# Kernel tuning notes

Measured on AMD Instinct MI355X. Metric: run time of the kernel, lower is better.

Reference implementation:

```python
import jax, jax.numpy as jnp
import numpy as np

IMG_TOK = 197  # hardcoded image/text split in the original module
BLOCK = 128


def setup_inputs() -> dict:
    key = jax.random.key(0)
    ks = jax.random.split(key, 11)
    B, Sk, Sv, D = 512, 128, 261, 768
    H, OUT = 58, 512
    return {
        "Q": jax.random.normal(ks[0], (B, D), jnp.float32),
        "K": jax.random.normal(ks[1], (B, Sk, D), jnp.float32),
        "V": jax.random.normal(ks[2], (B, Sv, D), jnp.float32),
        "Wq": jax.random.normal(ks[3], (H, D), jnp.float32) * 0.02,
        "bq": jax.random.normal(ks[4], (H,), jnp.float32) * 0.02,
        "Wk": jax.random.normal(ks[5], (H, D), jnp.float32) * 0.02,
        "bk": jax.random.normal(ks[6], (H,), jnp.float32) * 0.02,
        "Wsw": jax.random.normal(ks[7], (1, BLOCK), jnp.float32) * 0.02,
        "bsw": jax.random.normal(ks[8], (1,), jnp.float32) * 0.02,
        "Wv": jax.random.normal(ks[9], (OUT, D), jnp.float32) * 0.02,
        "bv": jax.random.normal(ks[10], (OUT,), jnp.float32) * 0.02,
    }


def reference(Q, K, V, Wq, bq, Wk, bk, Wsw, bsw, Wv, bv):
    Sk = K.shape[-2]
    # Linear projections (torch Linear: x @ W.T + b)
    Qt = Q[:, None, :] @ Wq.T + bq            # [B, 1, H]
    Kt = K @ Wk.T + bk                         # [B, Sk, H]
    Vt = V @ Wv.T + bv                         # [B, Sv, 512]
    # sigmoid attention over keys, scaled by sqrt(Sk)
    scores = jnp.einsum("bqh,bkh->bqk", Qt, Kt) / jnp.sqrt(jnp.float32(Sk))
    attn_weights = jax.nn.sigmoid(scores)      # [B, 1, Sk]
    # pad/truncate to BLOCK (no-op when Sk == BLOCK, matching original alignment)
    if attn_weights.shape[2] < BLOCK:
        attn_weights = jnp.pad(attn_weights, ((0, 0), (0, 0), (0, BLOCK - attn_weights.shape[2])))
    elif attn_weights.shape[2] > BLOCK:
        attn_weights = attn_weights[:, :, :BLOCK]
    # switch gate
    hot = jax.nn.sigmoid(attn_weights @ Wsw.T + bsw)   # [B, 1, 1]
    image_context = hot * Vt[:, :IMG_TOK, :]
    text_context = (1.0 - hot) * Vt[:, IMG_TOK:, :]
    context = jnp.concatenate((image_context, text_context), axis=1)  # [B, Sv, 512]
    return context, attn_weights
```

## Files before the change

kernel.cpp:

```cpp
#include <hip/hip_runtime.h>
#include <hip/hip_bf16.h>

constexpr int Bn   = 512;
constexpr int SK   = 128;
constexpr int SV   = 261;
constexpr int Dd   = 768;
constexpr int Hh   = 58;
constexpr int OUTn = 512;
constexpr int IMG  = 197;
constexpr int Mrows = Bn * SV;
constexpr long long CTX_ELEMS = (long long)Mrows * OUTn;

constexpr size_t WS_U   = 0;
constexpr size_t WS_C   = 1572864;
constexpr size_t WS_HOT = 1574912;
constexpr size_t WS_WB  = 1576960;

typedef __attribute__((ext_vector_type(8))) short short8;
typedef __attribute__((ext_vector_type(4))) float floatx4;

__device__ __forceinline__ short f2bf(float f) {
    return __builtin_bit_cast(short, __float2bfloat16(f));
}

__device__ __forceinline__ float sigmoidf_(float x) {
    return 1.0f / (1.0f + __expf(-x));
}

template <int N>
__device__ __forceinline__ void wait_vm() {
    asm volatile("s_waitcnt vmcnt(%0)" :: "n"(N) : "memory");
}

template <int OFF>
__device__ __forceinline__ floatx4 ds_read128(unsigned addr) {
    floatx4 r;
    asm volatile("ds_read_b128 %0, %1 offset:%2" : "=v"(r) : "v"(addr), "n"(OFF));
    return r;
}

__device__ __forceinline__ void lds_dma16(const float* src, float* dst) {
    __builtin_amdgcn_global_load_lds(
        (const __attribute__((address_space(1))) void*)src,
        (__attribute__((address_space(3))) void*)dst,
        16, 0, 0);
}

__global__ void __launch_bounds__(256) qt_u_kernel(
    const float* __restrict__ Q, const float* __restrict__ Wq, const float* __restrict__ bq,
    const float* __restrict__ Wk, const float* __restrict__ bk,
    float* __restrict__ u, float* __restrict__ c)
{
    int b = blockIdx.x;
    int t = threadIdx.x, lane = t & 63, w = t >> 6;

    __shared__ float qrow[Dd];
    __shared__ float qt[Hh];

    for (int d = t; d < Dd; d += 256) qrow[d] = Q[b * Dd + d];
    __syncthreads();

    for (int h = w; h < Hh; h += 4) {
        const float* wr = Wq + (size_t)h * Dd;
        float s = 0.f;
        #pragma unroll
        for (int j = 0; j < 12; ++j) { int d = lane + 64 * j; s += qrow[d] * wr[d]; }
        #pragma unroll
        for (int off = 32; off; off >>= 1) s += __shfl_down(s, off);
        if (lane == 0) qt[h] = s + bq[h];
    }
    __syncthreads();

    for (int d = t; d < Dd; d += 256) {
        float s = 0.f;
        #pragma unroll 2
        for (int h = 0; h < Hh; ++h) s += qt[h] * Wk[(size_t)h * Dd + d];
        u[(size_t)b * Dd + d] = s;
    }

    if (w == 0) {
        float v = (lane < Hh) ? qt[lane] * bk[lane] : 0.f;
        #pragma unroll
        for (int off = 32; off; off >>= 1) v += __shfl_down(v, off);
        if (lane == 0) c[b] = v;
    }
}

__global__ void __launch_bounds__(512) scores_kernel(
    const float* __restrict__ K, const float* __restrict__ u, const float* __restrict__ c,
    const float* __restrict__ Wsw, const float* __restrict__ bsw,
    float* __restrict__ attn_out, float* __restrict__ hot)
{
    int b = blockIdx.x;
    int t = threadIdx.x, lane = t & 63, w = t >> 6;

    __shared__ float ul[Dd];
    __shared__ float al[SK];

    for (int d = t; d < Dd; d += 512) ul[d] = u[(size_t)b * Dd + d];
    float cb = c[b];
    __syncthreads();

    const float* Kb = K + (size_t)b * SK * Dd;
    for (int k = w; k < SK; k += 8) {
        const float* kr = Kb + (size_t)k * Dd;
        float s = 0.f;
        #pragma unroll
        for (int j = 0; j < 12; ++j) { int d = lane + 64 * j; s += kr[d] * ul[d]; }
        #pragma unroll
        for (int off = 32; off; off >>= 1) s += __shfl_down(s, off);
        if (lane == 0) {
            float sc = (s + cb) * 0.0883883476483184f;
            float a = sigmoidf_(sc);
            attn_out[(size_t)b * SK + k] = a;
            al[k] = a;
        }
    }
    __syncthreads();

    if (w == 0) {
        float v = al[lane] * Wsw[lane] + al[lane + 64] * Wsw[lane + 64];
        #pragma unroll
        for (int off = 32; off; off >>= 1) v += __shfl_down(v, off);
        if (lane == 0) hot[b] = sigmoidf_(v + bsw[0]);
    }
}

__global__ void __launch_bounds__(256) wv_convert(
    const float* __restrict__ Wv, unsigned short* __restrict__ wsB)
{
    int t = blockIdx.x * 256 + threadIdx.x;
    if (t >= OUTn * Dd) return;
    int col = t / Dd;
    int k   = t - col * Dd;
    int kb = k >> 5, kgrp = (k >> 3) & 3, kj = k & 7;
    int g = col >> 4, cl = col & 15;
    size_t off = ((size_t)(kb * 32 + g) * 64 + (kgrp * 16 + cl)) * 8 + kj;
    wsB[off] = (unsigned short)f2bf(Wv[t]);
}

__global__ void __launch_bounds__(256, 2) ctx_gemm(
    const float* __restrict__ V, const unsigned short* __restrict__ wsB,
    const float* __restrict__ bv, const float* __restrict__ hot,
    float* __restrict__ out)
{
    int bid = blockIdx.x;
    int nt = bid & 1;
    int mt = bid >> 1;
    int t = threadIdx.x, lane = t & 63, w = t >> 6;
    int m_base = mt * 64;

    __shared__ float ldsA[3][2048];

    int r8 = lane >> 3;
    int glog = (lane & 7) ^ r8;
    const float* srcJ0 = V + (size_t)(m_base + w * 16 + r8) * Dd + glog * 4;
    const float* srcJ1 = srcJ0 + (size_t)8 * Dd;
    const int rb0 = (w * 16) * 32;
    const int rb1 = (w * 16 + 8) * 32;

    __attribute__((address_space(3))) float* l3 =
        (__attribute__((address_space(3))) float*)&ldsA[0][0];
    unsigned ldsBase = (unsigned)(unsigned long long)l3;
    int r0 = lane & 15;
    int g0 = (lane >> 4) * 2;
    unsigned adr0[4], adr1[4];
    #pragma unroll
    for (int mr = 0; mr < 4; ++mr) {
        int row = mr * 16 + r0;
        adr0[mr] = ldsBase + row * 128 + (unsigned)((g0 ^ (row & 7)) << 4);
        adr1[mr] = ldsBase + row * 128 + (unsigned)(((g0 + 1) ^ (row & 7)) << 4);
    }

    const unsigned short* bB = wsB + ((size_t)(nt * 16 + w * 4) * 64 + lane) * 8;

    floatx4 acc[4][4] = {};
    short8 pbA[4], pbB[4];

    lds_dma16(srcJ0, &ldsA[0][rb0]);
    lds_dma16(srcJ1, &ldsA[0][rb1]);
    lds_dma16(srcJ0 + 32, &ldsA[1][rb0]);
    lds_dma16(srcJ1 + 32, &ldsA[1][rb1]);
    #pragma unroll
    for (int nr = 0; nr < 4; ++nr) pbA[nr] = *(const short8*)(bB + (size_t)nr * 512);
    wait_vm<6>();
    __builtin_amdgcn_s_barrier();

#define KSTEP(T, BUF, PBC, PBN, VM, DOSTAGE, DOLOADB)                              \
  {                                                                                \
    if (DOSTAGE) {                                                                 \
      lds_dma16(srcJ0 + (size_t)((T) + 2) * 32, &ldsA[((T) + 2) % 3][rb0]);        \
      lds_dma16(srcJ1 + (size_t)((T) + 2) * 32, &ldsA[((T) + 2) % 3][rb1]);        \
    }                                                                              \
    __builtin_amdgcn_sched_barrier(0);                                             \
    if (DOLOADB) {                                                                 \
      _Pragma("unroll")                                                            \
      for (int nr = 0; nr < 4; ++nr)                                               \
        PBN[nr] = *(const short8*)(bB + ((size_t)((T) + 1) * 32 + nr) * 512);      \
    }                                                                              \
    __builtin_amdgcn_sched_barrier(0);                                             \
    floatx4 fr[8];                                                                 \
    _Pragma("unroll")                                                              \
    for (int mr = 0; mr < 4; ++mr) {                                               \
      fr[2 * mr]     = ds_read128<(BUF) * 8192>(adr0[mr]);                         \
      fr[2 * mr + 1] = ds_read128<(BUF) * 8192>(adr1[mr]);                         \
    }                                                                              \
    asm volatile("s_waitcnt lgkmcnt(0)" ::: "memory");                             \
    __builtin_amdgcn_sched_barrier(0);                                             \
    short8 af[4];                                                                  \
    _Pragma("unroll")                                                              \
    for (int mr = 0; mr < 4; ++mr) {                                               \
      floatx4 f0 = fr[2 * mr], f1 = fr[2 * mr + 1];                                \
      af[mr][0] = f2bf(f0[0]); af[mr][1] = f2bf(f0[1]);                            \
      af[mr][2] = f2bf(f0[2]); af[mr][3] = f2bf(f0[3]);                            \
      af[mr][4] = f2bf(f1[0]); af[mr][5] = f2bf(f1[1]);                            \
      af[mr][6] = f2bf(f1[2]); af[mr][7] = f2bf(f1[3]);                            \
    }                                                                              \
    wait_vm<VM>();                                                                 \
    __builtin_amdgcn_sched_barrier(0);                                             \
    _Pragma("unroll")                                                              \
    for (int mr = 0; mr < 4; ++mr) {                                               \
      _Pragma("unroll")                                                            \
      for (int nr = 0; nr < 4; ++nr)                                               \
        acc[mr][nr] = __builtin_amdgcn_mfma_f32_16x16x32_bf16(af[mr], PBC[nr],     \
                                                              acc[mr][nr], 0, 0, 0);\
    }                                                                              \
    __builtin_amdgcn_s_barrier();                                                  \
  }

    for (int tb = 0; tb < 3; ++tb) {
        int T0 = tb * 6;
        KSTEP(T0 + 0, 0, pbA, pbB, 6, 1, 1)
        KSTEP(T0 + 1, 1, pbB, pbA, 6, 1, 1)
        KSTEP(T0 + 2, 2, pbA, pbB, 6, 1, 1)
        KSTEP(T0 + 3, 0, pbB, pbA, 6, 1, 1)
        KSTEP(T0 + 4, 1, pbA, pbB, 6, 1, 1)
        KSTEP(T0 + 5, 2, pbB, pbA, 6, 1, 1)
    }
    KSTEP(18, 0, pbA, pbB, 6, 1, 1)
    KSTEP(19, 1, pbB, pbA, 6, 1, 1)
    KSTEP(20, 2, pbA, pbB, 6, 1, 1)
    KSTEP(21, 0, pbB, pbA, 6, 1, 1)
    KSTEP(22, 1, pbA, pbB, 4, 0, 1)
    KSTEP(23, 2, pbB, pbA, 0, 0, 0)
#undef KSTEP

    float bvv[4];
    #pragma unroll
    for (int nr = 0; nr < 4; ++nr)
        bvv[nr] = bv[nt * 256 + w * 64 + nr * 16 + (lane & 15)];

    int ncol0 = nt * 256 + w * 64 + (lane & 15);
    #pragma unroll
    for (int mr = 0; mr < 4; ++mr) {
        #pragma unroll
        for (int rg = 0; rg < 4; ++rg) {
            int m = m_base + mr * 16 + ((lane >> 4) << 2) + rg;
            int b = m / 261;
            int s = m - b * 261;
            float h = hot[b];
            float scale = (s < IMG) ? h : (1.0f - h);
            float* orow = out + (size_t)m * OUTn + ncol0;
            #pragma unroll
            for (int nr = 0; nr < 4; ++nr)
                orow[nr * 16] = scale * (acc[mr][nr][rg] + bvv[nr]);
        }
    }
}

extern "C" void kernel_launch(void* const* d_in, const int* in_sizes, int n_in,
                              void* d_out, int out_size, void* d_ws, size_t ws_size,
                              hipStream_t stream) {
    const float* Q   = (const float*)d_in[0];
    const float* K   = (const float*)d_in[1];
    const float* V   = (const float*)d_in[2];
    const float* Wq  = (const float*)d_in[3];
    const float* bq  = (const float*)d_in[4];
    const float* Wk  = (const float*)d_in[5];
    const float* bk  = (const float*)d_in[6];
    const float* Wsw = (const float*)d_in[7];
    const float* bsw = (const float*)d_in[8];
    const float* Wv  = (const float*)d_in[9];
    const float* bv  = (const float*)d_in[10];

    float* out = (float*)d_out;
    char* ws = (char*)d_ws;
    float* u   = (float*)(ws + WS_U);
    float* c   = (float*)(ws + WS_C);
    float* hot = (float*)(ws + WS_HOT);
    unsigned short* wsB = (unsigned short*)(ws + WS_WB);

    hipLaunchKernelGGL(wv_convert, dim3((OUTn * Dd + 255) / 256), dim3(256), 0, stream, Wv, wsB);
    hipLaunchKernelGGL(qt_u_kernel, dim3(Bn), dim3(256), 0, stream, Q, Wq, bq, Wk, bk, u, c);
    hipLaunchKernelGGL(scores_kernel, dim3(Bn), dim3(512), 0, stream,
                       K, u, c, Wsw, bsw, out + CTX_ELEMS, hot);
    hipLaunchKernelGGL(ctx_gemm, dim3((Mrows / 64) * 2), dim3(256), 0, stream, V, wsB, bv, hot, out);
}
```

Baseline: 327.5 us.

## Fuse query projection into scores kernel and deepen GEMM A-tile pipeline

Merges the qt/u projection kernel into the scores kernel, so u and c stay in LDS instead of going through global workspace, and vectorizes its dot products with float4 loads. The context GEMM moves from a 3-stage to a 4-stage LDS prefetch ring, prefetching three K-steps ahead with adjusted wait counts. It also raises the occupancy hint to 3 blocks per CU and remaps block IDs with a stride-522 interleave to change which tiles run together. The extra LDS stage and higher occupancy target may put pressure on registers and LDS capacity.

```diff
diff --git a/kernel.cpp b/kernel.cpp
--- a/kernel.cpp
+++ b/kernel.cpp
@@ -11,10 +11,8 @@
 constexpr int Mrows = Bn * SV;
 constexpr long long CTX_ELEMS = (long long)Mrows * OUTn;
 
-constexpr size_t WS_U   = 0;
-constexpr size_t WS_C   = 1572864;
-constexpr size_t WS_HOT = 1574912;
-constexpr size_t WS_WB  = 1576960;
+constexpr size_t WS_HOT = 0;
+constexpr size_t WS_WB  = 4096;
 
 typedef __attribute__((ext_vector_type(8))) short short8;
 typedef __attribute__((ext_vector_type(4))) float floatx4;
@@ -46,67 +44,66 @@
         16, 0, 0);
 }
 
-__global__ void __launch_bounds__(256) qt_u_kernel(
-    const float* __restrict__ Q, const float* __restrict__ Wq, const float* __restrict__ bq,
+__global__ void __launch_bounds__(512) scores_fused(
+    const float* __restrict__ Q, const float* __restrict__ K,
+    const float* __restrict__ Wq, const float* __restrict__ bq,
     const float* __restrict__ Wk, const float* __restrict__ bk,
-    float* __restrict__ u, float* __restrict__ c)
-{
-    int b = blockIdx.x;
-    int t = threadIdx.x, lane = t & 63, w = t >> 6;
-
-    __shared__ float qrow[Dd];
-    __shared__ float qt[Hh];
-
-    for (int d = t; d < Dd; d += 256) qrow[d] = Q[b * Dd + d];
-    __syncthreads();
-
-    for (int h = w; h < Hh; h += 4) {
-        const float* wr = Wq + (size_t)h * Dd;
-        float s = 0.f;
-        #pragma unroll
-        for (int j = 0; j < 12; ++j) { int d = lane + 64 * j; s += qrow[d] * wr[d]; }
-        #pragma unroll
-        for (int off = 32; off; off >>= 1) s += __shfl_down(s, off);
-        if (lane == 0) qt[h] = s + bq[h];
-    }
-    __syncthreads();
-
-    for (int d = t; d < Dd; d += 256) {
-        float s = 0.f;
-        #pragma unroll 2
-        for (int h = 0; h < Hh; ++h) s += qt[h] * Wk[(size_t)h * Dd + d];
-        u[(size_t)b * Dd + d] = s;
-    }
-
-    if (w == 0) {
-        float v = (lane < Hh) ? qt[lane] * bk[lane] : 0.f;
-        #pragma unroll
-        for (int off = 32; off; off >>= 1) v += __shfl_down(v, off);
-        if (lane == 0) c[b] = v;
-    }
-}
-
-__global__ void __launch_bounds__(512) scores_kernel(
-    const float* __restrict__ K, const float* __restrict__ u, const float* __restrict__ c,
     const float* __restrict__ Wsw, const float* __restrict__ bsw,
     float* __restrict__ attn_out, float* __restrict__ hot)
 {
     int b = blockIdx.x;
     int t = threadIdx.x, lane = t & 63, w = t >> 6;
 
-    __shared__ float ul[Dd];
+    __shared__ __align__(16) float qrow[Dd];
+    __shared__ float qt[64];
+    __shared__ __align__(16) float ul[Dd];
     __shared__ float al[SK];
-
-    for (int d = t; d < Dd; d += 512) ul[d] = u[(size_t)b * Dd + d];
-    float cb = c[b];
+    __shared__ float cbs;
+
+    qrow[t] = Q[b * Dd + t];
+    if (t < Dd - 512) qrow[t + 512] = Q[b * Dd + t + 512];
     __syncthreads();
 
-    const float* Kb = K + (size_t)b * SK * Dd;
+    for (int h = w; h < Hh; h += 8) {
+        const float4* wr4 = (const float4*)(Wq + (size_t)h * Dd);
+        const float4* q4  = (const float4*)qrow;
+        float s = 0.f;
+        #pragma unroll
+        for (int j = 0; j < 3; ++j) {
+            float4 a = q4[lane + 64 * j], c = wr4[lane + 64 * j];
+            s += a.x * c.x + a.y * c.y + a.z * c.z + a.w * c.w;
+        }
+        #pragma unroll
+        for (int off = 32; off; off >>= 1) s += __shfl_down(s, off);
+        if (lane == 0) qt[h] = s + bq[h];
+    }
+    __syncthreads();
+
+    for (int d = t; d < Dd; d += 512) {
+        float s = 0.f;
+        #pragma unroll 2
+        for (int h = 0; h < Hh; ++h) s += qt[h] * Wk[(size_t)h * Dd + d];
+        ul[d] = s;
+    }
+    if (w == 0) {
+        float v = (lane < Hh) ? qt[lane] * bk[lane] : 0.f;
+        #pragma unroll
+        for (int off = 32; off; off >>= 1) v += __shfl_down(v, off);
+        if (lane == 0) cbs = v;
+    }
+    __syncthreads();
+
+    float cb = cbs;
+    const float4* Kb4 = (const float4*)(K + (size_t)b * SK * Dd);
+    const float4* u4  = (const float4*)ul;
     for (int k = w; k < SK; k += 8) {
-        const float* kr = Kb + (size_t)k * Dd;
+        const float4* kr4 = Kb4 + (size_t)k * (Dd / 4);
         float s = 0.f;
         #pragma unroll
-        for (int j = 0; j < 12; ++j) { int d = lane + 64 * j; s += kr[d] * ul[d]; }
+        for (int j = 0; j < 3; ++j) {
+            float4 a = kr4[lane + 64 * j], c = u4[lane + 64 * j];
+            s += a.x * c.x + a.y * c.y + a.z * c.z + a.w * c.w;
+        }
         #pragma unroll
         for (int off = 32; off; off >>= 1) s += __shfl_down(s, off);
         if (lane == 0) {
@@ -139,18 +136,18 @@
     wsB[off] = (unsigned short)f2bf(Wv[t]);
 }
 
-__global__ void __launch_bounds__(256, 2) ctx_gemm(
+__global__ void __launch_bounds__(256, 3) ctx_gemm(
     const float* __restrict__ V, const unsigned short* __restrict__ wsB,
     const float* __restrict__ bv, const float* __restrict__ hot,
     float* __restrict__ out)
 {
-    int bid = blockIdx.x;
+    int bid = (blockIdx.x >> 3) + (blockIdx.x & 7) * 522;
     int nt = bid & 1;
     int mt = bid >> 1;
     int t = threadIdx.x, lane = t & 63, w = t >> 6;
     int m_base = mt * 64;
 
-    __shared__ float ldsA[3][2048];
+    __shared__ float ldsA[4][2048];
 
     int r8 = lane >> 3;
     int glog = (lane & 7) ^ r8;
@@ -181,29 +178,31 @@
     lds_dma16(srcJ1, &ldsA[0][rb1]);
     lds_dma16(srcJ0 + 32, &ldsA[1][rb0]);
     lds_dma16(srcJ1 + 32, &ldsA[1][rb1]);
+    lds_dma16(srcJ0 + 64, &ldsA[2][rb0]);
+    lds_dma16(srcJ1 + 64, &ldsA[2][rb1]);
     #pragma unroll
     for (int nr = 0; nr < 4; ++nr) pbA[nr] = *(const short8*)(bB + (size_t)nr * 512);
-    wait_vm<6>();
+    wait_vm<8>();
     __builtin_amdgcn_s_barrier();
 
-#define KSTEP(T, BUF, PBC, PBN, VM, DOSTAGE, DOLOADB)                              \
+#define KSTEP(T, PBC, PBN, VM, DOSTAGE, DOLOADB)                                   \
   {                                                                                \
-    if (DOSTAGE) {                                                                 \
-      lds_dma16(srcJ0 + (size_t)((T) + 2) * 32, &ldsA[((T) + 2) % 3][rb0]);        \
-      lds_dma16(srcJ1 + (size_t)((T) + 2) * 32, &ldsA[((T) + 2) % 3][rb1]);        \
-    }                                                                              \
-    __builtin_amdgcn_sched_barrier(0);                                             \
     if (DOLOADB) {                                                                 \
       _Pragma("unroll")                                                            \
       for (int nr = 0; nr < 4; ++nr)                                               \
         PBN[nr] = *(const short8*)(bB + ((size_t)((T) + 1) * 32 + nr) * 512);      \
     }                                                                              \
     __builtin_amdgcn_sched_barrier(0);                                             \
+    if (DOSTAGE) {                                                                 \
+      lds_dma16(srcJ0 + (size_t)((T) + 3) * 32, &ldsA[((T) + 3) & 3][rb0]);        \
+      lds_dma16(srcJ1 + (size_t)((T) + 3) * 32, &ldsA[((T) + 3) & 3][rb1]);        \
+    }                                                                              \
+    __builtin_amdgcn_sched_barrier(0);                                             \
     floatx4 fr[8];                                                                 \
     _Pragma("unroll")                                                              \
     for (int mr = 0; mr < 4; ++mr) {                                               \
-      fr[2 * mr]     = ds_read128<(BUF) * 8192>(adr0[mr]);                         \
-      fr[2 * mr + 1] = ds_read128<(BUF) * 8192>(adr1[mr]);                         \
+      fr[2 * mr]     = ds_read128<((T) & 3) * 8192>(adr0[mr]);                     \
+      fr[2 * mr + 1] = ds_read128<((T) & 3) * 8192>(adr1[mr]);                     \
     }                                                                              \
     asm volatile("s_waitcnt lgkmcnt(0)" ::: "memory");                             \
     __builtin_amdgcn_sched_barrier(0);                                             \
@@ -228,21 +227,30 @@
     __builtin_amdgcn_s_barrier();                                                  \
   }
 
-    for (int tb = 0; tb < 3; ++tb) {
-        int T0 = tb * 6;
-        KSTEP(T0 + 0, 0, pbA, pbB, 6, 1, 1)
-        KSTEP(T0 + 1, 1, pbB, pbA, 6, 1, 1)
-        KSTEP(T0 + 2, 2, pbA, pbB, 6, 1, 1)
-        KSTEP(T0 + 3, 0, pbB, pbA, 6, 1, 1)
-        KSTEP(T0 + 4, 1, pbA, pbB, 6, 1, 1)
-        KSTEP(T0 + 5, 2, pbB, pbA, 6, 1, 1)
-    }
-    KSTEP(18, 0, pbA, pbB, 6, 1, 1)
-    KSTEP(19, 1, pbB, pbA, 6, 1, 1)
-    KSTEP(20, 2, pbA, pbB, 6, 1, 1)
-    KSTEP(21, 0, pbB, pbA, 6, 1, 1)
-    KSTEP(22, 1, pbA, pbB, 4, 0, 1)
-    KSTEP(23, 2, pbB, pbA, 0, 0, 0)
+    KSTEP(0,  pbA, pbB, 6, 1, 1)
+    KSTEP(1,  pbB, pbA, 8, 1, 1)
+    KSTEP(2,  pbA, pbB, 8, 1, 1)
+    KSTEP(3,  pbB, pbA, 8, 1, 1)
+    KSTEP(4,  pbA, pbB, 8, 1, 1)
+    KSTEP(5,  pbB, pbA, 8, 1, 1)
+    KSTEP(6,  pbA, pbB, 8, 1, 1)
+    KSTEP(7,  pbB, pbA, 8, 1, 1)
+    KSTEP(8,  pbA, pbB, 8, 1, 1)
+    KSTEP(9,  pbB, pbA, 8, 1, 1)
+    KSTEP(10, pbA, pbB, 8, 1, 1)
+    KSTEP(11, pbB, pbA, 8, 1, 1)
+    KSTEP(12, pbA, pbB, 8, 1, 1)
+    KSTEP(13, pbB, pbA, 8, 1, 1)
+    KSTEP(14, pbA, pbB, 8, 1, 1)
+    KSTEP(15, pbB, pbA, 8, 1, 1)
+    KSTEP(16, pbA, pbB, 8, 1, 1)
+    KSTEP(17, pbB, pbA, 8, 1, 1)
+    KSTEP(18, pbA, pbB, 8, 1, 1)
+    KSTEP(19, pbB, pbA, 8, 1, 1)
+    KSTEP(20, pbA, pbB, 8, 1, 1)
+    KSTEP(21, pbB, pbA, 6, 0, 1)
+    KSTEP(22, pbA, pbB, 4, 0, 1)
+    KSTEP(23, pbB, pbA, 0, 0, 0)
 #undef KSTEP
 
     float bvv[4];
@@ -285,14 +293,11 @@
 
     float* out = (float*)d_out;
     char* ws = (char*)d_ws;
-    float* u   = (float*)(ws + WS_U);
-    float* c   = (float*)(ws + WS_C);
     float* hot = (float*)(ws + WS_HOT);
     unsigned short* wsB = (unsigned short*)(ws + WS_WB);
 
     hipLaunchKernelGGL(wv_convert, dim3((OUTn * Dd + 255) / 256), dim3(256), 0, stream, Wv, wsB);
-    hipLaunchKernelGGL(qt_u_kernel, dim3(Bn), dim3(256), 0, stream, Q, Wq, bq, Wk, bk, u, c);
-    hipLaunchKernelGGL(scores_kernel, dim3(Bn), dim3(512), 0, stream,
-                       K, u, c, Wsw, bsw, out + CTX_ELEMS, hot);
+    hipLaunchKernelGGL(scores_fused, dim3(Bn), dim3(512), 0, stream,
+                       Q, K, Wq, bq, Wk, bk, Wsw, bsw, out + CTX_ELEMS, hot);
     hipLaunchKernelGGL(ctx_gemm, dim3((Mrows / 64) * 2), dim3(256), 0, stream, V, wsB, bv, hot, out);
 }
```

Result: faster. 298.7 us (-8.8%).
